# Performance work log

Hardware: AMD Instinct MI355X
Metric: run time of the kernel (lower is better)

The kernel has to match this reference:

```python
import jax, jax.numpy as jnp
import numpy as np

S, D, H = 2048, 2048, 16
HD = D // H  # head dim = 128
LN_EPS = 1e-5


def _ln(x, g, b):
    mu = jnp.mean(x, axis=-1, keepdims=True)
    var = jnp.var(x, axis=-1, keepdims=True)
    return (x - mu) / jnp.sqrt(var + LN_EPS) * g + b


def setup_inputs() -> dict:
    key = jax.random.key(0)
    ks = jax.random.split(key, 8)
    B = 2
    s = 0.02  # weight init scale
    return {
        "x": jax.random.normal(ks[0], (B, S, D), jnp.float32),
        "Wq": jax.random.normal(ks[1], (D, D), jnp.float32) * s,
        "bq": jnp.zeros((D,), jnp.float32),
        "Wk": jax.random.normal(ks[2], (D, D), jnp.float32) * s,
        "bk": jnp.zeros((D,), jnp.float32),
        "Wv": jax.random.normal(ks[3], (D, D), jnp.float32) * s,
        "bv": jnp.zeros((D,), jnp.float32),
        "Wo": jax.random.normal(ks[4], (D, D), jnp.float32) * s,
        "bo": jnp.zeros((D,), jnp.float32),
        "ln1_g": jnp.ones((D,), jnp.float32),
        "ln1_b": jnp.zeros((D,), jnp.float32),
        "ln2_g": jnp.ones((D,), jnp.float32),
        "ln2_b": jnp.zeros((D,), jnp.float32),
        "W1": jax.random.normal(ks[5], (4 * D, D), jnp.float32) * s,
        "b1": jnp.zeros((4 * D,), jnp.float32),
        "W2": jax.random.normal(ks[6], (D, 4 * D), jnp.float32) * s,
        "b2": jnp.zeros((D,), jnp.float32),
    }


def reference(x, Wq, bq, Wk, bk, Wv, bv, Wo, bo,
              ln1_g, ln1_b, ln2_g, ln2_b, W1, b1, W2, b2):
    causal = jnp.tril(jnp.ones((S, S), bool))  # [S, S] lower-triangular mask
    neg = jnp.finfo(x.dtype).min
    inv_sqrt_hd = 1.0 / jnp.sqrt(jnp.asarray(HD, x.dtype))

    def block(xs):  # xs: [S, D] (equinox module is per-sequence; vmapped over batch)
        h = _ln(xs, ln1_g, ln1_b)
        q = (h @ Wq.T + bq).reshape(S, H, HD)
        k = (h @ Wk.T + bk).reshape(S, H, HD)
        v = (h @ Wv.T + bv).reshape(S, H, HD)
        logits = jnp.einsum('shd,Shd->hsS', q, k) * inv_sqrt_hd
        logits = jnp.where(causal, logits, neg)
        attn = jax.nn.softmax(logits, axis=-1)
        o = jnp.einsum('hsS,Shd->shd', attn, v).reshape(S, D)
        h = h + (o @ Wo.T + bo)          # residual of post-ln1 value (as in source)
        h2 = _ln(h, ln2_g, ln2_b)
        m = jax.nn.gelu(h2 @ W1.T + b1) @ W2.T + b2
        return h2 + m                    # residual of post-ln2 value (as in source)

    return jax.vmap(block)(x)
```

## Files before the change

### kernel.cpp

```cpp
#include <hip/hip_runtime.h>
#include <hip/hip_bf16.h>
#include <math.h>

#define DD   2048
#define SS   2048
#define HH   16
#define HDIM 128
#define BB   2
#define MM   4096
#define D4   8192

using bf16x8 = __attribute__((ext_vector_type(8))) short;
using f32x4  = __attribute__((ext_vector_type(4))) float;
using f32x16 = __attribute__((ext_vector_type(16))) float;

__device__ __forceinline__ ushort f2bf(float x) {
  uint u = __builtin_bit_cast(uint, x);
  u += 0x7FFFu + ((u >> 16) & 1u);
  return (ushort)(u >> 16);
}

__device__ __forceinline__ float gelu_f(float v) {
  float u = 0.7978845608028654f * (v + 0.044715f * v * v * v);
  float e = __expf(2.0f * u);
  float th = 1.0f - 2.0f / (e + 1.0f);
  return 0.5f * v * (1.0f + th);
}

__device__ __forceinline__ void gload_lds16(const void* g, void* l) {
  __builtin_amdgcn_global_load_lds(
      (const __attribute__((address_space(1))) void*)g,
      (__attribute__((address_space(3))) void*)l, 16, 0, 0);
}

__global__ __launch_bounds__(256) void cvt_f32_bf16(
    const float* __restrict__ in, ushort* __restrict__ out, int n4) {
  int i = blockIdx.x * 256 + threadIdx.x;
  if (i >= n4) return;
  float4 v = ((const float4*)in)[i];
  ushort4 o;
  o.x = f2bf(v.x); o.y = f2bf(v.y); o.z = f2bf(v.z); o.w = f2bf(v.w);
  ((ushort4*)out)[i] = o;
}

__global__ __launch_bounds__(256) void ln_rows(
    const float* __restrict__ in, const float* __restrict__ gam,
    const float* __restrict__ bet, float* __restrict__ outf,
    ushort* __restrict__ outb) {
  int row = blockIdx.x;
  int t = threadIdx.x;
  const float4* r4 = (const float4*)(in + (size_t)row * DD);
  float4 v0 = r4[t], v1 = r4[t + 256];
  float s = v0.x + v0.y + v0.z + v0.w + v1.x + v1.y + v1.z + v1.w;
  __shared__ float redA[4], redB[4];
  #pragma unroll
  for (int off = 32; off >= 1; off >>= 1) s += __shfl_xor(s, off);
  if ((t & 63) == 0) redA[t >> 6] = s;
  __syncthreads();
  float mean = (redA[0] + redA[1] + redA[2] + redA[3]) * (1.0f / DD);
  float d0 = v0.x - mean, d1 = v0.y - mean, d2 = v0.z - mean, d3 = v0.w - mean;
  float d4 = v1.x - mean, d5 = v1.y - mean, d6 = v1.z - mean, d7 = v1.w - mean;
  float q = d0*d0 + d1*d1 + d2*d2 + d3*d3 + d4*d4 + d5*d5 + d6*d6 + d7*d7;
  #pragma unroll
  for (int off = 32; off >= 1; off >>= 1) q += __shfl_xor(q, off);
  if ((t & 63) == 0) redB[t >> 6] = q;
  __syncthreads();
  float var = (redB[0] + redB[1] + redB[2] + redB[3]) * (1.0f / DD);
  float rstd = rsqrtf(var + 1e-5f);
  const float4* g4 = (const float4*)gam;
  const float4* b4 = (const float4*)bet;
  float4 g0 = g4[t], g1 = g4[t + 256], bb0 = b4[t], bb1 = b4[t + 256];
  float4 y0, y1;
  y0.x = d0 * rstd * g0.x + bb0.x;  y0.y = d1 * rstd * g0.y + bb0.y;
  y0.z = d2 * rstd * g0.z + bb0.z;  y0.w = d3 * rstd * g0.w + bb0.w;
  y1.x = d4 * rstd * g1.x + bb1.x;  y1.y = d5 * rstd * g1.y + bb1.y;
  y1.z = d6 * rstd * g1.z + bb1.z;  y1.w = d7 * rstd * g1.w + bb1.w;
  float4* of4 = (float4*)(outf + (size_t)row * DD);
  of4[t] = y0; of4[t + 256] = y1;
  ushort4 u0, u1;
  u0.x = f2bf(y0.x); u0.y = f2bf(y0.y); u0.z = f2bf(y0.z); u0.w = f2bf(y0.w);
  u1.x = f2bf(y1.x); u1.y = f2bf(y1.y); u1.z = f2bf(y1.z); u1.w = f2bf(y1.w);
  ushort4* ob4 = (ushort4*)(outb + (size_t)row * DD);
  ob4[t] = u0; ob4[t + 256] = u1;
}

template <int OMODE, bool GELU_, bool RES_>
__global__ __launch_bounds__(512, 2) void gemm2(
    const ushort* __restrict__ A, const ushort* __restrict__ Bt,
    const float* __restrict__ bias, const float* __restrict__ res,
    void* __restrict__ Cout, int M, int N, int K) {
  extern __shared__ __align__(16) ushort smem[];
  const int nbm = M >> 8, nbn = N >> 7;
  const int nwg = nbm * nbn;
  int wg = blockIdx.x;
  int wg2 = (wg & 7) * (nwg >> 3) + (wg >> 3);
  int bm = wg2 % nbm, bn = wg2 / nbm;
  int m0 = bm << 8, n0 = bn << 7;
  int t = threadIdx.x, lane = t & 63, w = t >> 6;
  int wm = w >> 2, wn = w & 3;
  int lr = lane & 15, lg = lane >> 4;

  auto stage = [&](int kt, int slot) {
    int k0 = kt << 6;
    ushort* lA = smem + slot * 24576;
    ushort* lB = lA + 16384;
    #pragma unroll
    for (int r = 0; r < 4; r++) {
      int idx = (r << 9) + t;
      int row = idx >> 3, ch = idx & 7;
      gload_lds16(A + (size_t)(m0 + row) * K + k0 + ((ch ^ (row & 7)) << 3),
                  lA + idx * 8);
    }
    #pragma unroll
    for (int r = 0; r < 2; r++) {
      int idx = (r << 9) + t;
      int row = idx >> 3, ch = idx & 7;
      gload_lds16(Bt + (size_t)(n0 + row) * K + k0 + ((ch ^ (row & 7)) << 3),
                  lB + idx * 8);
    }
  };

  f32x4 acc[8][2] = {};
  const int NT = K >> 6;
  stage(0, 0);
  stage(1, 1);
  int slot = 0;
  for (int kt = 0; kt < NT; ++kt) {
    __builtin_amdgcn_sched_barrier(0);
    if (kt + 1 < NT)
      asm volatile("s_waitcnt vmcnt(6) lgkmcnt(0)" ::: "memory");
    else
      asm volatile("s_waitcnt vmcnt(0) lgkmcnt(0)" ::: "memory");
    __builtin_amdgcn_s_barrier();
    __builtin_amdgcn_sched_barrier(0);
    if (kt + 2 < NT) {
      int s2 = slot + 2; if (s2 >= 3) s2 -= 3;
      stage(kt + 2, s2);
    }
    const ushort* lA = smem + slot * 24576;
    const ushort* lB = lA + 16384;
    bf16x8 af[8][2], bfr[2][2];
    #pragma unroll
    for (int mi = 0; mi < 8; mi++) {
      int row = wm * 128 + mi * 16 + lr;
      #pragma unroll
      for (int ks = 0; ks < 2; ks++)
        af[mi][ks] = *(const bf16x8*)
            &lA[row * 64 + (((ks * 4 + lg) ^ (row & 7)) << 3)];
    }
    #pragma unroll
    for (int ni = 0; ni < 2; ni++) {
      int row = wn * 32 + ni * 16 + lr;
      #pragma unroll
      for (int ks = 0; ks < 2; ks++)
        bfr[ni][ks] = *(const bf16x8*)
            &lB[row * 64 + (((ks * 4 + lg) ^ (row & 7)) << 3)];
    }
    __builtin_amdgcn_s_setprio(1);
    #pragma unroll
    for (int ks = 0; ks < 2; ks++)
      #pragma unroll
      for (int mi = 0; mi < 8; mi++)
        #pragma unroll
        for (int ni = 0; ni < 2; ni++)
          acc[mi][ni] = __builtin_amdgcn_mfma_f32_16x16x32_bf16(
              af[mi][ks], bfr[ni][ks], acc[mi][ni], 0, 0, 0);
    __builtin_amdgcn_s_setprio(0);
    slot = (slot + 1 == 3) ? 0 : slot + 1;
  }

  float bv[2];
  #pragma unroll
  for (int ni = 0; ni < 2; ni++) bv[ni] = bias[n0 + wn * 32 + ni * 16 + lr];

  if (OMODE == 2) {
    #pragma unroll
    for (int mi = 0; mi < 8; mi++) {
      int mg = m0 + wm * 128 + mi * 16 + lg * 4;
      int bb_ = mg >> 11, sb = mg & 2047;
      #pragma unroll
      for (int ni = 0; ni < 2; ni++) {
        int n = n0 + wn * 32 + ni * 16 + lr;
        ushort4 u4;
        u4.x = f2bf(acc[mi][ni][0] + bv[ni]);
        u4.y = f2bf(acc[mi][ni][1] + bv[ni]);
        u4.z = f2bf(acc[mi][ni][2] + bv[ni]);
        u4.w = f2bf(acc[mi][ni][3] + bv[ni]);
        size_t idx = ((size_t)((bb_ << 4) | (n >> 7)) * 128 + (n & 127)) * 2048
                     + sb;
        *(ushort4*)&((ushort*)Cout)[idx] = u4;
      }
    }
    return;
  }

  #pragma unroll
  for (int mi = 0; mi < 8; mi++) {
    #pragma unroll
    for (int r = 0; r < 4; r++) {
      int m = m0 + wm * 128 + mi * 16 + lg * 4 + r;
      #pragma unroll
      for (int ni = 0; ni < 2; ni++) {
        int n = n0 + wn * 32 + ni * 16 + lr;
        size_t idx = (size_t)m * N + n;
        float v = acc[mi][ni][r] + bv[ni];
        if (RES_) v += res[idx];
        if (GELU_) v = gelu_f(v);
        if (OMODE == 1) ((ushort*)Cout)[idx] = f2bf(v);
        else            ((float*)Cout)[idx] = v;
      }
    }
  }
}

__global__ __launch_bounds__(256) void attn_fwd(
    const ushort* __restrict__ qb, const ushort* __restrict__ kb,
    const ushort* __restrict__ vTb, ushort* __restrict__ ob) {
  __shared__ ushort Ks[64 * 128];
  __shared__ ushort Vs[128 * 64];
  __shared__ ushort Ps[4][32 * 64];

  int blk = blockIdx.x;
  int i15 = blk & 15;
  int qt = (blk & 256) ? i15 : 15 - i15;
  int bh = blk >> 4;
  int b = bh >> 4, h = bh & 15;
  int q0 = qt << 7;
  int t = threadIdx.x, lane = t & 63, w = t >> 6;
  int l31 = lane & 31, hi = lane >> 5;
  const size_t base = (size_t)b * SS * DD + (size_t)h * HDIM;
  const ushort* qp = qb + base;
  const ushort* kp = kb + base;
  const ushort* vp = vTb + (size_t)bh * HDIM * SS;
  int wq0 = q0 + w * 32;
  int qg = wq0 + l31;

  bf16x8 qf[8];
  #pragma unroll
  for (int kk = 0; kk < 8; kk++)
    qf[kk] = *(const bf16x8*)(qp + (size_t)qg * DD + kk * 16 + hi * 8);

  f32x16 o[4] = {};
  float mu = -1e30f, lrow = 0.f;
  const float csc = 0.08838834764831845f * 1.4426950408889634f;

  int nIter = 2 * qt + 2;
  for (int it = 0; it < nIter; ++it) {
    int kv0 = it * 64;
    #pragma unroll
    for (int ii = 0; ii < 4; ii++) {
      int chunk = ii * 256 + t;
      int row = chunk >> 4, cc = chunk & 15;
      gload_lds16(kp + (size_t)(kv0 + row) * DD + ((cc ^ (row & 15)) << 3),
                  &Ks[chunk * 8]);
    }
    #pragma unroll
    for (int ii = 0; ii < 4; ii++) {
      int chunk = ii * 256 + t;
      int row = chunk >> 3, cc = chunk & 7;
      gload_lds16(vp + (size_t)row * SS + kv0 + ((cc ^ (row & 7)) << 3),
                  &Vs[chunk * 8]);
    }
    __syncthreads();

    if (kv0 <= wq0 + 31) {
      f32x16 s2[2] = {};
      #pragma unroll
      for (int nt = 0; nt < 2; nt++) {
        int row = nt * 32 + l31;
        #pragma unroll
        for (int kk = 0; kk < 8; kk++) {
          bf16x8 kf = *(const bf16x8*)
              &Ks[row * 128 + (((kk * 2 + hi) ^ (row & 15)) << 3)];
          s2[nt] = __builtin_amdgcn_mfma_f32_32x32x16_bf16(kf, qf[kk], s2[nt],
                                                           0, 0, 0);
        }
      }
      float mx = -3e38f;
      #pragma unroll
      for (int nt = 0; nt < 2; nt++) {
        #pragma unroll
        for (int r = 0; r < 16; r++) {
          int kvl = nt * 32 + (r & 3) + 8 * (r >> 2) + 4 * hi;
          float u = (kv0 + kvl > qg) ? -3e38f : s2[nt][r] * csc;
          s2[nt][r] = u;
          mx = fmaxf(mx, u);
        }
      }
      mx = fmaxf(mx, __shfl_xor(mx, 32));
      float mnew = fmaxf(mu, mx);
      float fr = exp2f(mu - mnew);
      mu = mnew;
      float sum = 0.f;
      #pragma unroll
      for (int nt = 0; nt < 2; nt++)
        #pragma unroll
        for (int r = 0; r < 16; r++) {
          float p = exp2f(s2[nt][r] - mnew);
          s2[nt][r] = p;
          sum += p;
        }
      sum += __shfl_xor(sum, 32);
      lrow = lrow * fr + sum;
      #pragma unroll
      for (int dt = 0; dt < 4; dt++)
        #pragma unroll
        for (int r = 0; r < 16; r++) o[dt][r] *= fr;
      #pragma unroll
      for (int nt = 0; nt < 2; nt++) {
        #pragma unroll
        for (int g2 = 0; g2 < 4; g2++) {
          ushort4 u4;
          u4.x = f2bf(s2[nt][g2 * 4 + 0]);
          u4.y = f2bf(s2[nt][g2 * 4 + 1]);
          u4.z = f2bf(s2[nt][g2 * 4 + 2]);
          u4.w = f2bf(s2[nt][g2 * 4 + 3]);
          int cp = (nt * 4 + g2) ^ (l31 & 7);
          *(ushort4*)&Ps[w][l31 * 64 + cp * 8 + hi * 4] = u4;
        }
      }
      asm volatile("s_waitcnt lgkmcnt(0)" ::: "memory");
      #pragma unroll
      for (int kk = 0; kk < 4; kk++) {
        bf16x8 pf = *(const bf16x8*)
            &Ps[w][l31 * 64 + (((kk * 2 + hi) ^ (l31 & 7)) << 3)];
        #pragma unroll
        for (int dt = 0; dt < 4; dt++) {
          int drow = dt * 32 + l31;
          bf16x8 vf = *(const bf16x8*)
              &Vs[drow * 64 + (((kk * 2 + hi) ^ (drow & 7)) << 3)];
          o[dt] = __builtin_amdgcn_mfma_f32_32x32x16_bf16(vf, pf, o[dt],
                                                          0, 0, 0);
        }
      }
    }
    __syncthreads();
  }

  float inv = 1.0f / lrow;
  #pragma unroll
  for (int dt = 0; dt < 4; dt++) {
    #pragma unroll
    for (int g2 = 0; g2 < 4; g2++) {
      ushort4 u4;
      u4.x = f2bf(o[dt][g2 * 4 + 0] * inv);
      u4.y = f2bf(o[dt][g2 * 4 + 1] * inv);
      u4.z = f2bf(o[dt][g2 * 4 + 2] * inv);
      u4.w = f2bf(o[dt][g2 * 4 + 3] * inv);
      int d = dt * 32 + 8 * g2 + 4 * hi;
      *(ushort4*)&ob[base + (size_t)qg * DD + d] = u4;
    }
  }
}

extern "C" void kernel_launch(void* const* d_in, const int* in_sizes, int n_in,
                              void* d_out, int out_size, void* d_ws,
                              size_t ws_size, hipStream_t stream) {
  const float* x    = (const float*)d_in[0];
  const float* Wq   = (const float*)d_in[1];
  const float* bq   = (const float*)d_in[2];
  const float* Wk   = (const float*)d_in[3];
  const float* bk   = (const float*)d_in[4];
  const float* Wv   = (const float*)d_in[5];
  const float* bv   = (const float*)d_in[6];
  const float* Wo   = (const float*)d_in[7];
  const float* bo   = (const float*)d_in[8];
  const float* ln1g = (const float*)d_in[9];
  const float* ln1b = (const float*)d_in[10];
  const float* ln2g = (const float*)d_in[11];
  const float* ln2b = (const float*)d_in[12];
  const float* W1   = (const float*)d_in[13];
  const float* b1   = (const float*)d_in[14];
  const float* W2   = (const float*)d_in[15];
  const float* b2   = (const float*)d_in[16];

  char* ws = (char*)d_ws;
  ushort* Wqb = (ushort*)(ws);
  ushort* Wkb = Wqb + (size_t)DD * DD;
  ushort* Wvb = Wkb + (size_t)DD * DD;
  ushort* Wob = Wvb + (size_t)DD * DD;
  ushort* W1b = (ushort*)(ws);
  ushort* W2b = W1b + (size_t)D4 * DD;
  ushort* qbf = (ushort*)(ws + 67108864);
  ushort* kbf = qbf + (size_t)MM * DD;
  ushort* vTt = kbf + (size_t)MM * DD;
  ushort* aob = vTt + (size_t)MM * DD;
  ushort* gb  = (ushort*)(ws + 67108864);
  float* hf  = (float*)(ws + 134217728);
  float* h2f = hf;
  ushort* hb  = (ushort*)(ws + 167772160);
  ushort* h2b = hb;
  float* h2in = (float*)(ws + 184549376);
  float* out  = (float*)d_out;

  const int LDSB = 147456;
  hipFuncSetAttribute((const void*)gemm2<1, false, false>,
                      hipFuncAttributeMaxDynamicSharedMemorySize, LDSB);
  hipFuncSetAttribute((const void*)gemm2<2, false, false>,
                      hipFuncAttributeMaxDynamicSharedMemorySize, LDSB);
  hipFuncSetAttribute((const void*)gemm2<0, false, true>,
                      hipFuncAttributeMaxDynamicSharedMemorySize, LDSB);
  hipFuncSetAttribute((const void*)gemm2<1, true, false>,
                      hipFuncAttributeMaxDynamicSharedMemorySize, LDSB);

  dim3 blk(256);
  dim3 gblk(512);
  cvt_f32_bf16<<<DD * DD / 4 / 256, blk, 0, stream>>>(Wq, Wqb, DD * DD / 4);
  cvt_f32_bf16<<<DD * DD / 4 / 256, blk, 0, stream>>>(Wk, Wkb, DD * DD / 4);
  cvt_f32_bf16<<<DD * DD / 4 / 256, blk, 0, stream>>>(Wv, Wvb, DD * DD / 4);
  cvt_f32_bf16<<<DD * DD / 4 / 256, blk, 0, stream>>>(Wo, Wob, DD * DD / 4);
  ln_rows<<<MM, blk, 0, stream>>>(x, ln1g, ln1b, hf, hb);
  gemm2<1, false, false><<<256, gblk, LDSB, stream>>>(hb, Wqb, bq, nullptr, qbf, MM, DD, DD);
  gemm2<1, false, false><<<256, gblk, LDSB, stream>>>(hb, Wkb, bk, nullptr, kbf, MM, DD, DD);
  gemm2<2, false, false><<<256, gblk, LDSB, stream>>>(hb, Wvb, bv, nullptr, vTt, MM, DD, DD);
  attn_fwd<<<512, blk, 0, stream>>>(qbf, kbf, vTt, aob);
  gemm2<0, false, true><<<256, gblk, LDSB, stream>>>(aob, Wob, bo, hf, h2in, MM, DD, DD);
  ln_rows<<<MM, blk, 0, stream>>>(h2in, ln2g, ln2b, h2f, h2b);
  cvt_f32_bf16<<<D4 * DD / 4 / 256, blk, 0, stream>>>(W1, W1b, D4 * DD / 4);
  cvt_f32_bf16<<<D4 * DD / 4 / 256, blk, 0, stream>>>(W2, W2b, D4 * DD / 4);
  gemm2<1, true, false><<<1024, gblk, LDSB, stream>>>(h2b, W1b, b1, nullptr, gb, MM, D4, DD);
  gemm2<0, false, true><<<256, gblk, LDSB, stream>>>(gb, W2b, b2, h2f, out, MM, DD, D4);
}
```

Before: 673.8 us.

## Split GEMM k-step into two half-tile phases interleaving loads with MFMA

The GEMM main loop is restructured so each k-tile runs in two phases. Each phase reads half of the A fragments from LDS, issues half of the next-next tile's global-to-LDS loads, and runs half of the MFMAs, with barriers between phases. The goal is to spread memory traffic across the MFMA work and lower register pressure by holding only four A fragments at a time. The cost is extra workgroup barriers per iteration and a more fragile wait-count schedule.

```diff
diff --git a/kernel.cpp b/kernel.cpp
--- a/kernel.cpp
+++ b/kernel.cpp
@@ -100,72 +100,112 @@
   int wm = w >> 2, wn = w & 3;
   int lr = lane & 15, lg = lane >> 4;
 
-  auto stage = [&](int kt, int slot) {
+  auto stageA = [&](int kt, int slot) {
     int k0 = kt << 6;
     ushort* lA = smem + slot * 24576;
     ushort* lB = lA + 16384;
     #pragma unroll
-    for (int r = 0; r < 4; r++) {
+    for (int r = 0; r < 2; r++) {
       int idx = (r << 9) + t;
       int row = idx >> 3, ch = idx & 7;
       gload_lds16(A + (size_t)(m0 + row) * K + k0 + ((ch ^ (row & 7)) << 3),
                   lA + idx * 8);
     }
-    #pragma unroll
-    for (int r = 0; r < 2; r++) {
+    { int idx = t, row = idx >> 3, ch = idx & 7;
+      gload_lds16(Bt + (size_t)(n0 + row) * K + k0 + ((ch ^ (row & 7)) << 3),
+                  lB + idx * 8); }
+  };
+  auto stageB = [&](int kt, int slot) {
+    int k0 = kt << 6;
+    ushort* lA = smem + slot * 24576;
+    ushort* lB = lA + 16384;
+    #pragma unroll
+    for (int r = 2; r < 4; r++) {
       int idx = (r << 9) + t;
       int row = idx >> 3, ch = idx & 7;
+      gload_lds16(A + (size_t)(m0 + row) * K + k0 + ((ch ^ (row & 7)) << 3),
+                  lA + idx * 8);
+    }
+    { int idx = 512 + t, row = idx >> 3, ch = idx & 7;
       gload_lds16(Bt + (size_t)(n0 + row) * K + k0 + ((ch ^ (row & 7)) << 3),
-                  lB + idx * 8);
-    }
+                  lB + idx * 8); }
   };
 
   f32x4 acc[8][2] = {};
   const int NT = K >> 6;
-  stage(0, 0);
-  stage(1, 1);
+  stageA(0, 0); stageB(0, 0);
+  stageA(1, 1); stageB(1, 1);
+  asm volatile("s_waitcnt vmcnt(6)" ::: "memory");
+  __builtin_amdgcn_s_barrier();
   int slot = 0;
   for (int kt = 0; kt < NT; ++kt) {
-    __builtin_amdgcn_sched_barrier(0);
-    if (kt + 1 < NT)
-      asm volatile("s_waitcnt vmcnt(6) lgkmcnt(0)" ::: "memory");
-    else
-      asm volatile("s_waitcnt vmcnt(0) lgkmcnt(0)" ::: "memory");
-    __builtin_amdgcn_s_barrier();
-    __builtin_amdgcn_sched_barrier(0);
-    if (kt + 2 < NT) {
-      int s2 = slot + 2; if (s2 >= 3) s2 -= 3;
-      stage(kt + 2, s2);
-    }
+    int sp2 = slot + 2; if (sp2 >= 3) sp2 -= 3;
     const ushort* lA = smem + slot * 24576;
     const ushort* lB = lA + 16384;
-    bf16x8 af[8][2], bfr[2][2];
-    #pragma unroll
-    for (int mi = 0; mi < 8; mi++) {
+    bf16x8 bfr[2][2], af[4][2];
+    #pragma unroll
+    for (int ni = 0; ni < 2; ni++) {
+      int row = wn * 32 + ni * 16 + lr;
+      #pragma unroll
+      for (int ks = 0; ks < 2; ks++)
+        bfr[ni][ks] = *(const bf16x8*)
+            &lB[row * 64 + (((ks * 4 + lg) ^ (row & 7)) << 3)];
+    }
+    #pragma unroll
+    for (int mi = 0; mi < 4; mi++) {
       int row = wm * 128 + mi * 16 + lr;
       #pragma unroll
       for (int ks = 0; ks < 2; ks++)
         af[mi][ks] = *(const bf16x8*)
             &lA[row * 64 + (((ks * 4 + lg) ^ (row & 7)) << 3)];
     }
-    #pragma unroll
-    for (int ni = 0; ni < 2; ni++) {
-      int row = wn * 32 + ni * 16 + lr;
-      #pragma unroll
-      for (int ks = 0; ks < 2; ks++)
-        bfr[ni][ks] = *(const bf16x8*)
-            &lB[row * 64 + (((ks * 4 + lg) ^ (row & 7)) << 3)];
-    }
+    if (kt + 2 < NT) stageA(kt + 2, sp2);
+    __builtin_amdgcn_sched_barrier(0);
+    __builtin_amdgcn_s_barrier();
+    asm volatile("s_waitcnt lgkmcnt(0)" ::: "memory");
+    __builtin_amdgcn_sched_barrier(0);
     __builtin_amdgcn_s_setprio(1);
     #pragma unroll
     for (int ks = 0; ks < 2; ks++)
       #pragma unroll
-      for (int mi = 0; mi < 8; mi++)
+      for (int mi = 0; mi < 4; mi++)
         #pragma unroll
         for (int ni = 0; ni < 2; ni++)
           acc[mi][ni] = __builtin_amdgcn_mfma_f32_16x16x32_bf16(
               af[mi][ks], bfr[ni][ks], acc[mi][ni], 0, 0, 0);
     __builtin_amdgcn_s_setprio(0);
+    __builtin_amdgcn_sched_barrier(0);
+    __builtin_amdgcn_s_barrier();
+    bf16x8 ag[4][2];
+    #pragma unroll
+    for (int mi = 0; mi < 4; mi++) {
+      int row = wm * 128 + 64 + mi * 16 + lr;
+      #pragma unroll
+      for (int ks = 0; ks < 2; ks++)
+        ag[mi][ks] = *(const bf16x8*)
+            &lA[row * 64 + (((ks * 4 + lg) ^ (row & 7)) << 3)];
+    }
+    if (kt + 2 < NT) stageB(kt + 2, sp2);
+    __builtin_amdgcn_sched_barrier(0);
+    if (kt + 2 < NT)
+      asm volatile("s_waitcnt vmcnt(6)" ::: "memory");
+    else if (kt + 1 < NT)
+      asm volatile("s_waitcnt vmcnt(0)" ::: "memory");
+    __builtin_amdgcn_s_barrier();
+    asm volatile("s_waitcnt lgkmcnt(0)" ::: "memory");
+    __builtin_amdgcn_sched_barrier(0);
+    __builtin_amdgcn_s_setprio(1);
+    #pragma unroll
+    for (int ks = 0; ks < 2; ks++)
+      #pragma unroll
+      for (int mi = 0; mi < 4; mi++)
+        #pragma unroll
+        for (int ni = 0; ni < 2; ni++)
+          acc[mi + 4][ni] = __builtin_amdgcn_mfma_f32_16x16x32_bf16(
+              ag[mi][ks], bfr[ni][ks], acc[mi + 4][ni], 0, 0, 0);
+    __builtin_amdgcn_s_setprio(0);
+    __builtin_amdgcn_sched_barrier(0);
+    __builtin_amdgcn_s_barrier();
     slot = (slot + 1 == 3) ? 0 : slot + 1;
   }
 
```

After: 696.6 us. 1.03x slower.
